# Optimization experiments

Measured on AMD Instinct MI355X. Metric: run time of the kernel, lower is better.

Reference implementation:

```python
import jax, jax.numpy as jnp
import numpy as np

N = 1048576        # batch
DTOT = 64          # total dims in u
D = 32             # transformed dims (len(nodes))
K = 40             # knots = num spline bins
B = 5.0            # tail bound: bins/2 = ceil(max|limit|)


def setup_inputs() -> dict:
    key = jax.random.key(0)
    k1, k2, k3, k4 = jax.random.split(key, 4)
    # scale inputs so they cover many bins and some fall in the identity tails
    u = jax.random.normal(k1, (N, DTOT), jnp.float32) * 3.0
    w = jax.random.uniform(k2, (D, K), jnp.float32, -0.5, 0.5)
    h = jax.random.uniform(k3, (D, K), jnp.float32, -0.5, 0.5)
    d = jax.random.uniform(k4, (D, K - 1), jnp.float32, -0.5, 0.5)
    nodes = jnp.arange(D, dtype=jnp.int32)
    return {"u": u, "w": w, "h": h, "d": d, "nodes": nodes}


def _rqs_forward(x, w, h, d):
    # x: [N, D] selected dims; w,h: [D, K]; d: [D, K-1]
    dt = x.dtype
    widths = jax.nn.softmax(w, axis=-1) * (2.0 * B)          # [D, K]
    cumw = jnp.concatenate(
        [jnp.full((D, 1), -B, dt), -B + jnp.cumsum(widths, -1)], -1)  # [D, K+1]
    heights = jax.nn.softmax(h, axis=-1) * (2.0 * B)
    cumh = jnp.concatenate(
        [jnp.full((D, 1), -B, dt), -B + jnp.cumsum(heights, -1)], -1)
    # interior derivatives via softplus, boundary derivatives fixed to 1 (linear tails)
    derivs = jnp.concatenate(
        [jnp.ones((D, 1), dt), jax.nn.softplus(d), jnp.ones((D, 1), dt)], -1)  # [D, K+1]

    inside = jnp.abs(x) <= B
    xc = jnp.clip(x, -B, B)
    # per-dim bin search (irregular, data-dependent)
    idx = jax.vmap(lambda kn, xd: jnp.searchsorted(kn, xd, side='right'))(cumw, xc.T).T - 1
    idx = jnp.clip(idx, 0, K - 1)                             # [N, D]

    dd = jnp.arange(D)[None, :]
    cw = cumw[dd, idx]; bw = widths[dd, idx]
    ch = cumh[dd, idx]; bh = heights[dd, idx]
    d0 = derivs[dd, idx]; d1 = derivs[dd, idx + 1]
    delta = bh / bw                                            # bin slope

    theta = (xc - cw) / bw
    t1m = theta * (1.0 - theta)
    denom = delta + (d0 + d1 - 2.0 * delta) * t1m
    num = bh * (delta * theta * theta + d0 * t1m)
    y = ch + num / denom
    logdet = (jnp.log(delta * delta * (d1 * theta * theta
                                       + 2.0 * delta * t1m
                                       + d0 * (1.0 - theta) ** 2))
              - 2.0 * jnp.log(denom))

    y = jnp.where(inside, y, x)                # identity tails
    logdet = jnp.where(inside, logdet, 0.0)
    return y, logdet.sum(-1)                   # [N, D], [N]


def reference(u, w, h, d, nodes):
    y, logd = _rqs_forward(u[:, nodes], w, h, d)
    x = u.at[:, nodes].set(y)
    return x, logd
```

## Files before the change

kernel.cpp:

```cpp
#include <hip/hip_runtime.h>
#include <math.h>

#define NROWS 1048576
#define DTOT  64
#define D     32
#define K     40
#define Bf    5.0f
#define G     128
#define GS    132
#define TP    (K + 1)

#define OFF_CUMW 0
#define OFF_DER  (D * (K + 1))
#define OFF_RBW  (2 * D * (K + 1))
#define OFF_CH   (2 * D * (K + 1) + D * K)
#define OFF_BH   (2 * D * (K + 1) + 2 * D * K)
#define OFF_GS_BYTES ((2 * D * (K + 1) + 3 * D * K) * 4)
#define WS_BYTES (OFF_GS_BYTES + D * G)

typedef float nt_f4 __attribute__((ext_vector_type(4)));

__device__ __forceinline__ float dpp_add(float v, const int ctrl) {
    int r;
    switch (ctrl) {
    case 0:  r = __builtin_amdgcn_update_dpp(0, __float_as_int(v), 0xB1,  0xF, 0xF, false); break;
    case 1:  r = __builtin_amdgcn_update_dpp(0, __float_as_int(v), 0x4E,  0xF, 0xF, false); break;
    default: r = __builtin_amdgcn_update_dpp(0, __float_as_int(v), 0x141, 0xF, 0xF, false); break;
    }
    return v + __int_as_float(r);
}

__global__ __launch_bounds__(64) void build_tables(
    const float* __restrict__ w, const float* __restrict__ h,
    const float* __restrict__ dk,
    float* __restrict__ cumw_g, float* __restrict__ der_g,
    float* __restrict__ rbw_g, float* __restrict__ ch_g,
    float* __restrict__ bh_g, unsigned char* __restrict__ gs_g)
{
    const int j = blockIdx.x;
    const int k = threadIdx.x;
    __shared__ float s_cumw[K + 1];

    float wv = (k < K) ? w[j * K + k] : -INFINITY;
    float hv = (k < K) ? h[j * K + k] : -INFINITY;
    float mw = wv, mh = hv;
    for (int m = 32; m > 0; m >>= 1) {
        mw = fmaxf(mw, __shfl_xor(mw, m));
        mh = fmaxf(mh, __shfl_xor(mh, m));
    }
    float ew = (k < K) ? __expf(wv - mw) : 0.f;
    float eh = (k < K) ? __expf(hv - mh) : 0.f;
    float sw = ew, sh = eh;
    for (int m = 32; m > 0; m >>= 1) {
        sw += __shfl_xor(sw, m);
        sh += __shfl_xor(sh, m);
    }
    float width  = ew / sw * (2.f * Bf);
    float height = eh / sh * (2.f * Bf);

    float iw = width, ih = height;
    for (int off = 1; off < 64; off <<= 1) {
        float a = __shfl_up(iw, off);
        float b = __shfl_up(ih, off);
        if (k >= off) { iw += a; ih += b; }
    }
    const float cw_k    = -Bf + (iw - width);
    const float ch_k    = -Bf + (ih - height);
    const float cw_next = -Bf + iw;

    if (k <= K) {
        float dv = 1.f;
        if (k > 0 && k < K) dv = log1pf(__expf(dk[j * (K - 1) + (k - 1)]));
        der_g[j * (K + 1) + k] = dv;
    }
    if (k < K) {
        cumw_g[j * (K + 1) + k] = cw_k;
        rbw_g[j * K + k] = 1.f / width;
        ch_g [j * K + k] = ch_k;
        bh_g [j * K + k] = height;
        s_cumw[k] = cw_k;
    }
    if (k == K - 1) {
        cumw_g[j * (K + 1) + K] = cw_next;
        s_cumw[K] = cw_next;
    }
    __syncthreads();

    for (int c = k; c < G; c += 64) {
        float L = -Bf + (2.f * Bf) * ((float)c / (float)G);
        int idx = 0;
        for (int m = 1; m < K; ++m)
            if (s_cumw[m] <= L) idx = m;
        gs_g[j * G + c] = (unsigned char)idx;
    }
}

__global__ __launch_bounds__(512, 6) void rqs_main(
    const float4* __restrict__ u4,
    const float* __restrict__ cumw_g, const float* __restrict__ der_g,
    const float* __restrict__ rbw_g, const float* __restrict__ ch_g,
    const float* __restrict__ bh_g, const unsigned char* __restrict__ gs_g,
    float4* __restrict__ x4, float* __restrict__ logd, int ntiles)
{
    __shared__ float4 s_sel[D * TP];
    __shared__ float4 s_bin[D * TP];
    __shared__ unsigned char s_gs[D * GS];

    const int t = threadIdx.x;
    for (int e = t; e < D * K; e += 512) {
        const int j = e / K, k = e - j * K;
        const float cw0 = cumw_g[j * (K + 1) + k];
        const float cw1 = cumw_g[j * (K + 1) + k + 1];
        const float rb0 = rbw_g[e];
        const float rb1 = (k < K - 1) ? rbw_g[e + 1] : 1.f;
        s_sel[j * TP + k] = make_float4(cw0, rb0, cw1, rb1);
        s_bin[j * TP + k] = make_float4(ch_g[e], bh_g[e],
                                        der_g[j * (K + 1) + k],
                                        der_g[j * (K + 1) + k + 1]);
    }
    for (int i = t; i < D * G / 4; i += 512) {
        const int r = i >> 5, wi = i & 31;
        *(uint32_t*)(s_gs + r * GS + wi * 4) = ((const uint32_t*)gs_g)[i];
    }
    __syncthreads();

    const int seg = t & 7;
    const int rl  = t >> 3;

    int tile = blockIdx.x;
    float4 vt = make_float4(0.f, 0.f, 0.f, 0.f);
    if (tile < ntiles) vt = u4[(tile * 64 + rl) * 16 + seg];

    for (; tile < ntiles; tile += gridDim.x) {
        const int row = tile * 64 + rl;

        const int next = tile + gridDim.x;
        float4 nt = make_float4(0.f, 0.f, 0.f, 0.f);
        if (next < ntiles) nt = u4[(next * 64 + rl) * 16 + seg];

        const float4 vp = u4[row * 16 + 8 + seg];

        float vv[4] = {vt.x, vt.y, vt.z, vt.w};
        float prod = 1.f;
#pragma unroll
        for (int c = 0; c < 4; ++c) {
            const int j = seg * 4 + c;
            const float x = vv[c];
            const bool inside = fabsf(x) <= Bf;
            const float xc = fminf(fmaxf(x, -Bf), Bf);

            int cell = (int)((xc + Bf) * (G / (2.f * Bf)));
            cell = min(cell, G - 1);
            int i = s_gs[j * GS + cell];

            const float4 s = s_sel[j * TP + i];
            const bool adv = (xc >= s.z) && (i < K - 1);
            const float cw  = adv ? s.z : s.x;
            const float rbw = adv ? s.w : s.y;
            i += adv;

            const float4 b = s_bin[j * TP + i];
            const float ch = b.x, bh = b.y, d0 = b.z, d1 = b.w;

            const float delta = bh * rbw;
            const float theta = (xc - cw) * rbw;
            const float omt   = 1.f - theta;
            const float t1m   = theta * omt;
            const float th2   = theta * theta;
            const float denom = fmaf(fmaf(-2.f, delta, d0 + d1), t1m, delta);
            const float num   = bh * fmaf(d0, t1m, delta * th2);
            const float rd    = __builtin_amdgcn_rcpf(denom);
            const float y     = fmaf(num, rd, ch);
            const float Ap    = fmaf(d1, th2,
                                 fmaf(2.f * delta, t1m, d0 * omt * omt));
            const float term  = delta * delta * Ap * (rd * rd);

            vv[c] = inside ? y : x;
            prod  = inside ? prod * term : prod;
        }
        nt_f4 outv; outv.x = vv[0]; outv.y = vv[1]; outv.z = vv[2]; outv.w = vv[3];
        __builtin_nontemporal_store(outv,
            reinterpret_cast<nt_f4*>(&x4[row * 16 + seg]));
        __builtin_nontemporal_store(*reinterpret_cast<const nt_f4*>(&vp),
            reinterpret_cast<nt_f4*>(&x4[row * 16 + 8 + seg]));

        float ld = __logf(prod);
        ld = dpp_add(ld, 0);
        ld = dpp_add(ld, 1);
        ld = dpp_add(ld, 2);
        if (seg == 0) __builtin_nontemporal_store(ld, &logd[row]);

        vt = nt;
    }
}

extern "C" void kernel_launch(void* const* d_in, const int* in_sizes, int n_in,
                              void* d_out, int out_size, void* d_ws, size_t ws_size,
                              hipStream_t stream) {
    const float* u  = (const float*)d_in[0];
    const float* w  = (const float*)d_in[1];
    const float* h  = (const float*)d_in[2];
    const float* dk = (const float*)d_in[3];

    float* ws   = (float*)d_ws;
    float* cumw = ws + OFF_CUMW;
    float* der  = ws + OFF_DER;
    float* rbw  = ws + OFF_RBW;
    float* ch   = ws + OFF_CH;
    float* bh   = ws + OFF_BH;
    unsigned char* gs = (unsigned char*)d_ws + OFF_GS_BYTES;

    float* xout = (float*)d_out;
    float* logd = (float*)d_out + (size_t)NROWS * DTOT;

    build_tables<<<D, 64, 0, stream>>>(w, h, dk, cumw, der, rbw, ch, bh, gs);

    const int ntiles = NROWS / 64;
    rqs_main<<<768, 512, 0, stream>>>((const float4*)u, cumw, der, rbw, ch, bh,
                                      gs, (float4*)xout, logd, ntiles);
}
```

Measured before the change: 465.8 us.

## Process two rows per thread with deeper prefetch and plain stores

Each thread now handles two rows per tile (128 rows per tile) and interleaves their spline evaluation for more independent work. Both the transformed and passthrough halves of the next tile are prefetched into registers. Nontemporal stores become regular stores, and launch bounds drop occupancy from 6 to 4 blocks per CU to leave room for the extra registers. The aim is more memory-level parallelism per thread, at the cost of lower occupancy and possible changes in cache behaviour from the normal stores.

```diff
diff --git a/kernel.cpp b/kernel.cpp
--- a/kernel.cpp
+++ b/kernel.cpp
@@ -17,8 +17,6 @@
 #define OFF_BH   (2 * D * (K + 1) + 2 * D * K)
 #define OFF_GS_BYTES ((2 * D * (K + 1) + 3 * D * K) * 4)
 #define WS_BYTES (OFF_GS_BYTES + D * G)
-
-typedef float nt_f4 __attribute__((ext_vector_type(4)));
 
 __device__ __forceinline__ float dpp_add(float v, const int ctrl) {
     int r;
@@ -95,7 +93,7 @@
     }
 }
 
-__global__ __launch_bounds__(512, 6) void rqs_main(
+__global__ __launch_bounds__(512, 4) void rqs_main(
     const float4* __restrict__ u4,
     const float* __restrict__ cumw_g, const float* __restrict__ der_g,
     const float* __restrict__ rbw_g, const float* __restrict__ ch_g,
@@ -128,69 +126,81 @@
     const int rl  = t >> 3;
 
     int tile = blockIdx.x;
-    float4 vt = make_float4(0.f, 0.f, 0.f, 0.f);
-    if (tile < ntiles) vt = u4[(tile * 64 + rl) * 16 + seg];
+    float4 vtA = make_float4(0.f, 0.f, 0.f, 0.f), vtB = vtA;
+    float4 vpA = vtA, vpB = vtA;
+    if (tile < ntiles) {
+        const int rA = tile * 128 + rl, rB = rA + 64;
+        vtA = u4[rA * 16 + seg];      vtB = u4[rB * 16 + seg];
+        vpA = u4[rA * 16 + 8 + seg];  vpB = u4[rB * 16 + 8 + seg];
+    }
 
     for (; tile < ntiles; tile += gridDim.x) {
-        const int row = tile * 64 + rl;
+        const int rA = tile * 128 + rl, rB = rA + 64;
 
         const int next = tile + gridDim.x;
-        float4 nt = make_float4(0.f, 0.f, 0.f, 0.f);
-        if (next < ntiles) nt = u4[(next * 64 + rl) * 16 + seg];
-
-        const float4 vp = u4[row * 16 + 8 + seg];
-
-        float vv[4] = {vt.x, vt.y, vt.z, vt.w};
-        float prod = 1.f;
+        float4 nA = make_float4(0.f, 0.f, 0.f, 0.f), nB = nA, npA = nA, npB = nA;
+        if (next < ntiles) {
+            const int qA = next * 128 + rl, qB = qA + 64;
+            nA  = u4[qA * 16 + seg];      nB  = u4[qB * 16 + seg];
+            npA = u4[qA * 16 + 8 + seg];  npB = u4[qB * 16 + 8 + seg];
+        }
+
+        float va[4] = {vtA.x, vtA.y, vtA.z, vtA.w};
+        float vb[4] = {vtB.x, vtB.y, vtB.z, vtB.w};
+        float prodA = 1.f, prodB = 1.f;
 #pragma unroll
         for (int c = 0; c < 4; ++c) {
             const int j = seg * 4 + c;
-            const float x = vv[c];
-            const bool inside = fabsf(x) <= Bf;
-            const float xc = fminf(fmaxf(x, -Bf), Bf);
-
-            int cell = (int)((xc + Bf) * (G / (2.f * Bf)));
-            cell = min(cell, G - 1);
-            int i = s_gs[j * GS + cell];
-
-            const float4 s = s_sel[j * TP + i];
-            const bool adv = (xc >= s.z) && (i < K - 1);
-            const float cw  = adv ? s.z : s.x;
-            const float rbw = adv ? s.w : s.y;
-            i += adv;
-
-            const float4 b = s_bin[j * TP + i];
-            const float ch = b.x, bh = b.y, d0 = b.z, d1 = b.w;
-
-            const float delta = bh * rbw;
-            const float theta = (xc - cw) * rbw;
-            const float omt   = 1.f - theta;
-            const float t1m   = theta * omt;
-            const float th2   = theta * theta;
-            const float denom = fmaf(fmaf(-2.f, delta, d0 + d1), t1m, delta);
-            const float num   = bh * fmaf(d0, t1m, delta * th2);
-            const float rd    = __builtin_amdgcn_rcpf(denom);
-            const float y     = fmaf(num, rd, ch);
-            const float Ap    = fmaf(d1, th2,
-                                 fmaf(2.f * delta, t1m, d0 * omt * omt));
-            const float term  = delta * delta * Ap * (rd * rd);
-
-            vv[c] = inside ? y : x;
-            prod  = inside ? prod * term : prod;
+#pragma unroll
+            for (int r = 0; r < 2; ++r) {
+                const float x = r ? vb[c] : va[c];
+                const bool inside = fabsf(x) <= Bf;
+                const float xc = fminf(fmaxf(x, -Bf), Bf);
+
+                int cell = (int)((xc + Bf) * (G / (2.f * Bf)));
+                cell = min(cell, G - 1);
+                int i = s_gs[j * GS + cell];
+
+                const float4 s = s_sel[j * TP + i];
+                const bool adv = (xc >= s.z) && (i < K - 1);
+                const float cw  = adv ? s.z : s.x;
+                const float rbw = adv ? s.w : s.y;
+                i += adv;
+
+                const float4 b = s_bin[j * TP + i];
+                const float ch = b.x, bh = b.y, d0 = b.z, d1 = b.w;
+
+                const float delta = bh * rbw;
+                const float theta = (xc - cw) * rbw;
+                const float omt   = 1.f - theta;
+                const float t1m   = theta * omt;
+                const float th2   = theta * theta;
+                const float denom = fmaf(fmaf(-2.f, delta, d0 + d1), t1m, delta);
+                const float num   = bh * fmaf(d0, t1m, delta * th2);
+                const float rd    = __builtin_amdgcn_rcpf(denom);
+                const float y     = fmaf(num, rd, ch);
+                const float Ap    = fmaf(d1, th2,
+                                     fmaf(2.f * delta, t1m, d0 * omt * omt));
+                const float term  = delta * delta * Ap * (rd * rd);
+
+                if (r) { vb[c] = inside ? y : x; prodB = inside ? prodB * term : prodB; }
+                else   { va[c] = inside ? y : x; prodA = inside ? prodA * term : prodA; }
+            }
         }
-        nt_f4 outv; outv.x = vv[0]; outv.y = vv[1]; outv.z = vv[2]; outv.w = vv[3];
-        __builtin_nontemporal_store(outv,
-            reinterpret_cast<nt_f4*>(&x4[row * 16 + seg]));
-        __builtin_nontemporal_store(*reinterpret_cast<const nt_f4*>(&vp),
-            reinterpret_cast<nt_f4*>(&x4[row * 16 + 8 + seg]));
-
-        float ld = __logf(prod);
-        ld = dpp_add(ld, 0);
-        ld = dpp_add(ld, 1);
-        ld = dpp_add(ld, 2);
-        if (seg == 0) __builtin_nontemporal_store(ld, &logd[row]);
-
-        vt = nt;
+
+        x4[rA * 16 + seg]     = make_float4(va[0], va[1], va[2], va[3]);
+        x4[rB * 16 + seg]     = make_float4(vb[0], vb[1], vb[2], vb[3]);
+        x4[rA * 16 + 8 + seg] = vpA;
+        x4[rB * 16 + 8 + seg] = vpB;
+
+        float ldA = __logf(prodA);
+        float ldB = __logf(prodB);
+        ldA = dpp_add(ldA, 0); ldB = dpp_add(ldB, 0);
+        ldA = dpp_add(ldA, 1); ldB = dpp_add(ldB, 1);
+        ldA = dpp_add(ldA, 2); ldB = dpp_add(ldB, 2);
+        if (seg == 0) { logd[rA] = ldA; logd[rB] = ldB; }
+
+        vtA = nA; vtB = nB; vpA = npA; vpB = npB;
     }
 }
 
@@ -215,7 +225,7 @@
 
     build_tables<<<D, 64, 0, stream>>>(w, h, dk, cumw, der, rbw, ch, bh, gs);
 
-    const int ntiles = NROWS / 64;
+    const int ntiles = NROWS / 128;
     rqs_main<<<768, 512, 0, stream>>>((const float4*)u, cumw, der, rbw, ch, bh,
                                       gs, (float4*)xout, logd, ntiles);
 }
```

Result: faster. 456.1 us (-2.1%).
